# Kernel tuning notes

Measured on AMD Instinct MI355X. Metric: run time of the kernel, lower is better.

## Reference

```python
import jax, jax.numpy as jnp
import numpy as np

UNITS = 16
OUTPUT_LEN = 25


def _gru_cell(inp, h, kernel, recurrent_kernel, bias):
    """Keras GRUCell with reset_after=True (default), z/r/h gate ordering."""
    b_i, b_r = bias[0], bias[1]
    x_proj = inp @ kernel + b_i                 # [B, 3U]
    h_proj = h @ recurrent_kernel + b_r         # [B, 3U]
    xz, xr, xh = jnp.split(x_proj, 3, axis=-1)
    rz, rr, rh = jnp.split(h_proj, 3, axis=-1)
    z = jax.nn.sigmoid(xz + rz)
    r = jax.nn.sigmoid(xr + rr)
    hh = jnp.tanh(xh + r * rh)
    h_new = z * h + (1.0 - z) * hh
    return h_new


def setup_inputs() -> dict:
    key = jax.random.key(0)
    k1, k2, k3, k4 = jax.random.split(key, 4)
    B = 524288
    x = jax.random.normal(k1, (B, UNITS), dtype=jnp.float32)
    kernel = jax.random.normal(k2, (UNITS, 3 * UNITS), dtype=jnp.float32) * 0.25
    recurrent_kernel = jax.random.normal(k3, (UNITS, 3 * UNITS), dtype=jnp.float32) * 0.25
    bias = jax.random.normal(k4, (2, 3 * UNITS), dtype=jnp.float32) * 0.1
    return {"x": x, "kernel": kernel, "recurrent_kernel": recurrent_kernel, "bias": bias}


def reference(x, kernel, recurrent_kernel, bias):
    # initial input = zeros_like(x), initial state = x; GRU output == new state,
    # and each step's output is fed back as the next step's input.
    def step(carry, _):
        inp, h = carry
        h_new = _gru_cell(inp, h, kernel, recurrent_kernel, bias)
        return (h_new, h_new), h_new

    init = (jnp.zeros_like(x), x)
    _, outs = jax.lax.scan(step, init, None, length=OUTPUT_LEN)  # [T, B, U]
    return jnp.transpose(outs, (1, 0, 2))  # [B, T, U]
```

## Files before the change

### kernel.cpp

```cpp
#include <hip/hip_runtime.h>


#define UNITS 16
#define STEPS 25
#define ROWS_PER_BLOCK 16
#define BLOCK_THREADS 256

__device__ __forceinline__ float fast_rcp(float x)  { return __builtin_amdgcn_rcpf(x); }
__device__ __forceinline__ float fast_exp2(float x) { return __builtin_amdgcn_exp2f(x); }

__device__ __forceinline__ float fast_sigmoid(float x) {
    return fast_rcp(1.0f + fast_exp2(x * -1.4426950408889634f));
}
__device__ __forceinline__ float fast_tanh(float x) {
    return 1.0f - 2.0f * fast_rcp(1.0f + fast_exp2(x * 2.8853900817779268f));
}

__global__ __launch_bounds__(BLOCK_THREADS, 4)
void gru_seq_kernel(const float* __restrict__ x,
                    const float* __restrict__ K,
                    const float* __restrict__ RK,
                    const float* __restrict__ bias,
                    float* __restrict__ out,
                    int B)
{
    __shared__ float lds_h[ROWS_PER_BLOCK * UNITS];

    const int tid = threadIdx.x;
    const int u   = tid & (UNITS - 1);
    const int g   = tid >> 4;
    const int row = blockIdx.x * ROWS_PER_BLOCK + g;
    const bool active = row < B;

    float* lds_grp = &lds_h[g * UNITS];

    const float bi_z = bias[u],          br_z = bias[48 + u];
    const float bi_r = bias[16 + u],     br_r = bias[48 + 16 + u];
    const float bi_h = bias[32 + u],     br_h = bias[48 + 32 + u];

    float h_my = active ? x[(size_t)row * UNITS + u] : 0.0f;

    float hrep[16];
    {
        lds_grp[u] = h_my;
        float4 a = ((const float4*)lds_grp)[0];
        float4 b = ((const float4*)lds_grp)[1];
        float4 c = ((const float4*)lds_grp)[2];
        float4 d = ((const float4*)lds_grp)[3];
        hrep[0]=a.x; hrep[1]=a.y; hrep[2]=a.z; hrep[3]=a.w;
        hrep[4]=b.x; hrep[5]=b.y; hrep[6]=b.z; hrep[7]=b.w;
        hrep[8]=c.x; hrep[9]=c.y; hrep[10]=c.z; hrep[11]=c.w;
        hrep[12]=d.x; hrep[13]=d.y; hrep[14]=d.z; hrep[15]=d.w;
    }

    float* op = out + (size_t)row * (STEPS * UNITS) + u;

    {
        float az = bi_z + br_z;
        float ar = bi_r + br_r;
        float ah = br_h;
        #pragma unroll
        for (int k = 0; k < 16; ++k) {
            float xk = hrep[k];
            az = fmaf(xk, RK[k*48 + u],      az);
            ar = fmaf(xk, RK[k*48 + 16 + u], ar);
            ah = fmaf(xk, RK[k*48 + 32 + u], ah);
        }
        float z  = fast_sigmoid(az);
        float r  = fast_sigmoid(ar);
        float hh = fast_tanh(fmaf(r, ah, bi_h));
        float hn = fmaf(z, h_my - hh, hh);
        if (active) op[0] = hn;
        h_my = hn;
    }

    float Wz[16], Wr[16], Wh[16], Uh[16];
    #pragma unroll
    for (int k = 0; k < 16; ++k) {
        Wz[k] = K[k*48 + u]      + RK[k*48 + u];
        Wr[k] = K[k*48 + 16 + u] + RK[k*48 + 16 + u];
        Wh[k] = K[k*48 + 32 + u];
        Uh[k] = RK[k*48 + 32 + u];
    }
    const float bz = bi_z + br_z;
    const float brr = bi_r + br_r;

    for (int t = 1; t < STEPS; ++t) {
        lds_grp[u] = h_my;
        float4 a = ((const float4*)lds_grp)[0];
        float4 b = ((const float4*)lds_grp)[1];
        float4 c = ((const float4*)lds_grp)[2];
        float4 d = ((const float4*)lds_grp)[3];
        hrep[0]=a.x; hrep[1]=a.y; hrep[2]=a.z; hrep[3]=a.w;
        hrep[4]=b.x; hrep[5]=b.y; hrep[6]=b.z; hrep[7]=b.w;
        hrep[8]=c.x; hrep[9]=c.y; hrep[10]=c.z; hrep[11]=c.w;
        hrep[12]=d.x; hrep[13]=d.y; hrep[14]=d.z; hrep[15]=d.w;

        float az = bz, ar = brr, axh = bi_h, arh = br_h;
        #pragma unroll
        for (int k = 0; k < 16; ++k) {
            float hk = hrep[k];
            az  = fmaf(hk, Wz[k], az);
            ar  = fmaf(hk, Wr[k], ar);
            axh = fmaf(hk, Wh[k], axh);
            arh = fmaf(hk, Uh[k], arh);
        }
        float z  = fast_sigmoid(az);
        float r  = fast_sigmoid(ar);
        float hh = fast_tanh(fmaf(r, arh, axh));
        float hn = fmaf(z, h_my - hh, hh);
        if (active) op[t * UNITS] = hn;
        h_my = hn;
    }
}

extern "C" void kernel_launch(void* const* d_in, const int* in_sizes, int n_in,
                              void* d_out, int out_size, void* d_ws, size_t ws_size,
                              hipStream_t stream) {
    const float* x    = (const float*)d_in[0];
    const float* K    = (const float*)d_in[1];
    const float* RK   = (const float*)d_in[2];
    const float* bias = (const float*)d_in[3];
    float* out = (float*)d_out;

    const int B = in_sizes[0] / UNITS;
    const int grid = (B + ROWS_PER_BLOCK - 1) / ROWS_PER_BLOCK;
    gru_seq_kernel<<<grid, BLOCK_THREADS, 0, stream>>>(x, K, RK, bias, out, B);
}
```

Measured before the change: 1.110 ms.

## Process four rows per thread group to amortize weight registers and raise ILP

Each 16-thread group now handles J=4 batch rows instead of one, reusing the per-thread Wz/Wr/Wh/Uh weight registers across four independent recurrences. This interleaves four FMA chains per step to raise instruction-level parallelism and cuts the number of blocks by a factor of four. LDS stride is padded to reduce bank conflicts, and launch bounds drop to 2 blocks/SM to allow the higher register usage, which risks lower occupancy.

```diff
diff --git a/kernel.cpp b/kernel.cpp
--- a/kernel.cpp
+++ b/kernel.cpp
@@ -3,8 +3,11 @@
 
 #define UNITS 16
 #define STEPS 25
-#define ROWS_PER_BLOCK 16
+#define J 4
+#define GROUPS 16
+#define ROWS_PER_BLOCK (GROUPS * J)
 #define BLOCK_THREADS 256
+#define GSTRIDE (J * UNITS + 4)
 
 __device__ __forceinline__ float fast_rcp(float x)  { return __builtin_amdgcn_rcpf(x); }
 __device__ __forceinline__ float fast_exp2(float x) { return __builtin_amdgcn_exp2f(x); }
@@ -16,7 +19,7 @@
     return 1.0f - 2.0f * fast_rcp(1.0f + fast_exp2(x * 2.8853900817779268f));
 }
 
-__global__ __launch_bounds__(BLOCK_THREADS, 4)
+__global__ __launch_bounds__(BLOCK_THREADS, 2)
 void gru_seq_kernel(const float* __restrict__ x,
                     const float* __restrict__ K,
                     const float* __restrict__ RK,
@@ -24,44 +27,55 @@
                     float* __restrict__ out,
                     int B)
 {
-    __shared__ float lds_h[ROWS_PER_BLOCK * UNITS];
+    __shared__ float lds_h[GROUPS * GSTRIDE];
 
     const int tid = threadIdx.x;
     const int u   = tid & (UNITS - 1);
     const int g   = tid >> 4;
-    const int row = blockIdx.x * ROWS_PER_BLOCK + g;
-    const bool active = row < B;
+    const int row0 = blockIdx.x * ROWS_PER_BLOCK + g * J;
 
-    float* lds_grp = &lds_h[g * UNITS];
+    float* lds_grp = &lds_h[g * GSTRIDE];
 
     const float bi_z = bias[u],          br_z = bias[48 + u];
     const float bi_r = bias[16 + u],     br_r = bias[48 + 16 + u];
     const float bi_h = bias[32 + u],     br_h = bias[48 + 32 + u];
 
-    float h_my = active ? x[(size_t)row * UNITS + u] : 0.0f;
-
-    float hrep[16];
-    {
-        lds_grp[u] = h_my;
-        float4 a = ((const float4*)lds_grp)[0];
-        float4 b = ((const float4*)lds_grp)[1];
-        float4 c = ((const float4*)lds_grp)[2];
-        float4 d = ((const float4*)lds_grp)[3];
-        hrep[0]=a.x; hrep[1]=a.y; hrep[2]=a.z; hrep[3]=a.w;
-        hrep[4]=b.x; hrep[5]=b.y; hrep[6]=b.z; hrep[7]=b.w;
-        hrep[8]=c.x; hrep[9]=c.y; hrep[10]=c.z; hrep[11]=c.w;
-        hrep[12]=d.x; hrep[13]=d.y; hrep[14]=d.z; hrep[15]=d.w;
+    bool  act[J];
+    float h_my[J];
+    #pragma unroll
+    for (int j = 0; j < J; ++j) {
+        const int r = row0 + j;
+        act[j]  = r < B;
+        h_my[j] = act[j] ? x[(size_t)r * UNITS + u] : 0.0f;
     }
 
-    float* op = out + (size_t)row * (STEPS * UNITS) + u;
+    float* op[J];
+    #pragma unroll
+    for (int j = 0; j < J; ++j)
+        op[j] = out + (size_t)(row0 + j) * (STEPS * UNITS) + u;
 
-    {
+    float hrep[J][16];
+
+    #pragma unroll
+    for (int j = 0; j < J; ++j) lds_grp[j * UNITS + u] = h_my[j];
+    #pragma unroll
+    for (int j = 0; j < J; ++j) {
+        const float4* p = (const float4*)&lds_grp[j * UNITS];
+        float4 a = p[0], b = p[1], c = p[2], d = p[3];
+        hrep[j][0]=a.x;  hrep[j][1]=a.y;  hrep[j][2]=a.z;  hrep[j][3]=a.w;
+        hrep[j][4]=b.x;  hrep[j][5]=b.y;  hrep[j][6]=b.z;  hrep[j][7]=b.w;
+        hrep[j][8]=c.x;  hrep[j][9]=c.y;  hrep[j][10]=c.z; hrep[j][11]=c.w;
+        hrep[j][12]=d.x; hrep[j][13]=d.y; hrep[j][14]=d.z; hrep[j][15]=d.w;
+    }
+
+    #pragma unroll
+    for (int j = 0; j < J; ++j) {
         float az = bi_z + br_z;
         float ar = bi_r + br_r;
         float ah = br_h;
         #pragma unroll
         for (int k = 0; k < 16; ++k) {
-            float xk = hrep[k];
+            float xk = hrep[j][k];
             az = fmaf(xk, RK[k*48 + u],      az);
             ar = fmaf(xk, RK[k*48 + 16 + u], ar);
             ah = fmaf(xk, RK[k*48 + 32 + u], ah);
@@ -69,9 +83,9 @@
         float z  = fast_sigmoid(az);
         float r  = fast_sigmoid(ar);
         float hh = fast_tanh(fmaf(r, ah, bi_h));
-        float hn = fmaf(z, h_my - hh, hh);
-        if (active) op[0] = hn;
-        h_my = hn;
+        float hn = fmaf(z, h_my[j] - hh, hh);
+        if (act[j]) op[j][0] = hn;
+        h_my[j] = hn;
     }
 
     float Wz[16], Wr[16], Wh[16], Uh[16];
@@ -82,35 +96,48 @@
         Wh[k] = K[k*48 + 32 + u];
         Uh[k] = RK[k*48 + 32 + u];
     }
-    const float bz = bi_z + br_z;
+    const float bz  = bi_z + br_z;
     const float brr = bi_r + br_r;
 
+    #pragma unroll 1
     for (int t = 1; t < STEPS; ++t) {
-        lds_grp[u] = h_my;
-        float4 a = ((const float4*)lds_grp)[0];
-        float4 b = ((const float4*)lds_grp)[1];
-        float4 c = ((const float4*)lds_grp)[2];
-        float4 d = ((const float4*)lds_grp)[3];
-        hrep[0]=a.x; hrep[1]=a.y; hrep[2]=a.z; hrep[3]=a.w;
-        hrep[4]=b.x; hrep[5]=b.y; hrep[6]=b.z; hrep[7]=b.w;
-        hrep[8]=c.x; hrep[9]=c.y; hrep[10]=c.z; hrep[11]=c.w;
-        hrep[12]=d.x; hrep[13]=d.y; hrep[14]=d.z; hrep[15]=d.w;
+        #pragma unroll
+        for (int j = 0; j < J; ++j) lds_grp[j * UNITS + u] = h_my[j];
+        #pragma unroll
+        for (int j = 0; j < J; ++j) {
+            const float4* p = (const float4*)&lds_grp[j * UNITS];
+            float4 a = p[0], b = p[1], c = p[2], d = p[3];
+            hrep[j][0]=a.x;  hrep[j][1]=a.y;  hrep[j][2]=a.z;  hrep[j][3]=a.w;
+            hrep[j][4]=b.x;  hrep[j][5]=b.y;  hrep[j][6]=b.z;  hrep[j][7]=b.w;
+            hrep[j][8]=c.x;  hrep[j][9]=c.y;  hrep[j][10]=c.z; hrep[j][11]=c.w;
+            hrep[j][12]=d.x; hrep[j][13]=d.y; hrep[j][14]=d.z; hrep[j][15]=d.w;
+        }
 
-        float az = bz, ar = brr, axh = bi_h, arh = br_h;
+        float az[J], ar[J], axh[J], arh[J];
+        #pragma unroll
+        for (int j = 0; j < J; ++j) { az[j]=bz; ar[j]=brr; axh[j]=bi_h; arh[j]=br_h; }
+
         #pragma unroll
         for (int k = 0; k < 16; ++k) {
-            float hk = hrep[k];
-            az  = fmaf(hk, Wz[k], az);
-            ar  = fmaf(hk, Wr[k], ar);
-            axh = fmaf(hk, Wh[k], axh);
-            arh = fmaf(hk, Uh[k], arh);
+            #pragma unroll
+            for (int j = 0; j < J; ++j) {
+                float hk = hrep[j][k];
+                az[j]  = fmaf(hk, Wz[k], az[j]);
+                ar[j]  = fmaf(hk, Wr[k], ar[j]);
+                axh[j] = fmaf(hk, Wh[k], axh[j]);
+                arh[j] = fmaf(hk, Uh[k], arh[j]);
+            }
         }
-        float z  = fast_sigmoid(az);
-        float r  = fast_sigmoid(ar);
-        float hh = fast_tanh(fmaf(r, arh, axh));
-        float hn = fmaf(z, h_my - hh, hh);
-        if (active) op[t * UNITS] = hn;
-        h_my = hn;
+
+        #pragma unroll
+        for (int j = 0; j < J; ++j) {
+            float z  = fast_sigmoid(az[j]);
+            float r  = fast_sigmoid(ar[j]);
+            float hh = fast_tanh(fmaf(r, arh[j], axh[j]));
+            float hn = fmaf(z, h_my[j] - hh, hh);
+            if (act[j]) op[j][t * UNITS] = hn;
+            h_my[j] = hn;
+        }
     }
 }
 
```

Result: no change. 1.108 ms (-0.2%).
